# Kernel tuning notes

Measured on AMD Instinct MI355X. Metric: run time of the kernel, lower is better.

The kernel has to match this reference:

```python
import jax, jax.numpy as jnp
import numpy as np

B, L = 4096, 2048
TIMESTEPS = 1000
BETA_START, BETA_END = 1e-4, 0.02


def setup_inputs() -> dict:
    key = jax.random.key(0)
    k0, k1, k2 = jax.random.split(key, 3)
    x_0 = jax.random.normal(k0, (B, L, 2), dtype=jnp.float32)
    t = jax.random.randint(k1, (B,), 0, TIMESTEPS)
    noise = jax.random.normal(k2, (B, L, 2), dtype=jnp.float32)
    return {"x_0": x_0, "t": t, "noise": noise}


def reference(x_0, t, noise):
    # Schedules exactly as in PathDDPM.__init__
    betas = jnp.linspace(BETA_START, BETA_END, TIMESTEPS, dtype=x_0.dtype)
    alphas_cumprod = jnp.cumprod(1.0 - betas)
    sqrt_alphas_cumprod = jnp.sqrt(alphas_cumprod)
    sqrt_one_minus_alphas_cumprod = jnp.sqrt(1.0 - alphas_cumprod)
    # q(x_t | x_0): gather per-sample scalars, broadcast over [L, 2]
    a = sqrt_alphas_cumprod[t][:, None, None]       # [B,1,1]
    s = sqrt_one_minus_alphas_cumprod[t][:, None, None]  # [B,1,1]
    x_t = a * x_0 + s * noise
    return (x_t, noise)
```

## Files before the change

### kernel.cpp

```cpp
#include <hip/hip_runtime.h>
#include <math.h>


#define TSTEPS 1000
#define BSTART 1e-4
#define BEND   0.02

__global__ void ddpm_schedule_kernel(float* __restrict__ ws) {
    const int lane = threadIdx.x;
    const int CHUNK = 16;
    const double step = (BEND - BSTART) / (double)(TSTEPS - 1);
    const int i0 = lane * CHUNK;

    double p = 1.0;
    for (int k = 0; k < CHUNK; ++k) {
        int i = i0 + k;
        if (i < TSTEPS) {
            double beta = BSTART + step * (double)i;
            p *= (1.0 - beta);
        }
    }
    double scan = p;
    #pragma unroll
    for (int off = 1; off < 64; off <<= 1) {
        double o = __shfl_up(scan, off);
        if (lane >= off) scan *= o;
    }
    double excl = __shfl_up(scan, 1);
    if (lane == 0) excl = 1.0;

    double run = excl;
    for (int k = 0; k < CHUNK; ++k) {
        int i = i0 + k;
        if (i < TSTEPS) {
            double beta = BSTART + step * (double)i;
            run *= (1.0 - beta);
            ws[i]          = (float)sqrt(run);
            ws[TSTEPS + i] = (float)sqrt(1.0 - run);
        }
    }
}

__global__ void __launch_bounds__(256)
ddpm_qsample_kernel(const float4* __restrict__ x0,
                    const int*    __restrict__ t,
                    const float4* __restrict__ nz,
                    float4*       __restrict__ out_xt,
                    float4*       __restrict__ out_nz,
                    const float*  __restrict__ ws,
                    int n4) {
    const float* __restrict__ sa = ws;
    const float* __restrict__ ss = ws + TSTEPS;
    const int stride = gridDim.x * blockDim.x;
    for (int i = blockIdx.x * blockDim.x + threadIdx.x; i < n4; i += stride) {
        const int b  = i >> 10;
        const int tb = t[b];
        const float a = sa[tb];
        const float s = ss[tb];
        const float4 x = x0[i];
        const float4 n = nz[i];
        float4 o;
        o.x = fmaf(a, x.x, s * n.x);
        o.y = fmaf(a, x.y, s * n.y);
        o.z = fmaf(a, x.z, s * n.z);
        o.w = fmaf(a, x.w, s * n.w);
        out_xt[i] = o;
        out_nz[i] = n;
    }
}

extern "C" void kernel_launch(void* const* d_in, const int* in_sizes, int n_in,
                              void* d_out, int out_size, void* d_ws, size_t ws_size,
                              hipStream_t stream) {
    const float* x0 = (const float*)d_in[0];
    const int*   t  = (const int*)  d_in[1];
    const float* nz = (const float*)d_in[2];
    float* out = (float*)d_out;
    float* ws  = (float*)d_ws;

    const int n  = 4096 * 2048 * 2;
    const int n4 = n / 4;

    ddpm_schedule_kernel<<<1, 64, 0, stream>>>(ws);
    ddpm_qsample_kernel<<<2048, 256, 0, stream>>>(
        (const float4*)x0, t, (const float4*)nz,
        (float4*)out, (float4*)(out + n), ws, n4);
}
```

Before: 51.16 us.

## Fuse schedule computation into qsample kernel with shared-memory tables and nontemporal stores

Removes the separate single-block schedule kernel: every block now recomputes the cumulative-product tables into shared memory with one wavefront, then runs a fixed 8-iteration unrolled loop. The per-sample index is made wave-uniform with readfirstlane, and outputs are written with nontemporal stores. The aim is to drop one kernel launch and the serialization between the two kernels, and to cut cache pollution on the streaming writes. In exchange each block redundantly runs a double-precision scan before any loads, and the loop bounds are hardcoded to the problem size.

```diff
diff --git a/kernel.cpp b/kernel.cpp
--- a/kernel.cpp
+++ b/kernel.cpp
@@ -6,66 +6,69 @@
 #define BSTART 1e-4
 #define BEND   0.02
 
-__global__ void ddpm_schedule_kernel(float* __restrict__ ws) {
-    const int lane = threadIdx.x;
-    const int CHUNK = 16;
-    const double step = (BEND - BSTART) / (double)(TSTEPS - 1);
-    const int i0 = lane * CHUNK;
+typedef float f4 __attribute__((ext_vector_type(4)));
 
-    double p = 1.0;
-    for (int k = 0; k < CHUNK; ++k) {
-        int i = i0 + k;
-        if (i < TSTEPS) {
-            double beta = BSTART + step * (double)i;
-            p *= (1.0 - beta);
+__global__ void __launch_bounds__(256) ddpm_fused_kernel(
+    const f4*  __restrict__ x0,
+    const int* __restrict__ t,
+    const f4*  __restrict__ nz,
+    f4*        __restrict__ out_xt,
+    f4*        __restrict__ out_nz)
+{
+    __shared__ float s_a[TSTEPS];
+    __shared__ float s_s[TSTEPS];
+
+    if (threadIdx.x < 64) {
+        const int lane = threadIdx.x;
+        const double step = (BEND - BSTART) / (double)(TSTEPS - 1);
+        const int i0 = lane * 16;
+
+        double p = 1.0;
+        #pragma unroll
+        for (int k = 0; k < 16; ++k) {
+            int i = i0 + k;
+            if (i < TSTEPS) p *= (1.0 - (BSTART + step * (double)i));
+        }
+        double scan = p;
+        #pragma unroll
+        for (int off = 1; off < 64; off <<= 1) {
+            double o = __shfl_up(scan, off);
+            if (lane >= off) scan *= o;
+        }
+        double excl = __shfl_up(scan, 1);
+        if (lane == 0) excl = 1.0;
+
+        double run = excl;
+        #pragma unroll
+        for (int k = 0; k < 16; ++k) {
+            int i = i0 + k;
+            if (i < TSTEPS) {
+                run *= (1.0 - (BSTART + step * (double)i));
+                s_a[i] = (float)sqrt(run);
+                s_s[i] = (float)sqrt(1.0 - run);
+            }
         }
     }
-    double scan = p;
+    __syncthreads();
+
+    const int base = blockIdx.x * 256 + threadIdx.x;
     #pragma unroll
-    for (int off = 1; off < 64; off <<= 1) {
-        double o = __shfl_up(scan, off);
-        if (lane >= off) scan *= o;
-    }
-    double excl = __shfl_up(scan, 1);
-    if (lane == 0) excl = 1.0;
+    for (int k = 0; k < 8; ++k) {
+        const int i = base + k * 524288;
+        const int b  = __builtin_amdgcn_readfirstlane(i >> 10);
+        const int tb = t[b];
+        const float a = s_a[tb];
+        const float s = s_s[tb];
 
-    double run = excl;
-    for (int k = 0; k < CHUNK; ++k) {
-        int i = i0 + k;
-        if (i < TSTEPS) {
-            double beta = BSTART + step * (double)i;
-            run *= (1.0 - beta);
-            ws[i]          = (float)sqrt(run);
-            ws[TSTEPS + i] = (float)sqrt(1.0 - run);
-        }
-    }
-}
-
-__global__ void __launch_bounds__(256)
-ddpm_qsample_kernel(const float4* __restrict__ x0,
-                    const int*    __restrict__ t,
-                    const float4* __restrict__ nz,
-                    float4*       __restrict__ out_xt,
-                    float4*       __restrict__ out_nz,
-                    const float*  __restrict__ ws,
-                    int n4) {
-    const float* __restrict__ sa = ws;
-    const float* __restrict__ ss = ws + TSTEPS;
-    const int stride = gridDim.x * blockDim.x;
-    for (int i = blockIdx.x * blockDim.x + threadIdx.x; i < n4; i += stride) {
-        const int b  = i >> 10;
-        const int tb = t[b];
-        const float a = sa[tb];
-        const float s = ss[tb];
-        const float4 x = x0[i];
-        const float4 n = nz[i];
-        float4 o;
+        const f4 x = x0[i];
+        const f4 n = nz[i];
+        f4 o;
         o.x = fmaf(a, x.x, s * n.x);
         o.y = fmaf(a, x.y, s * n.y);
         o.z = fmaf(a, x.z, s * n.z);
         o.w = fmaf(a, x.w, s * n.w);
-        out_xt[i] = o;
-        out_nz[i] = n;
+        __builtin_nontemporal_store(o, &out_xt[i]);
+        __builtin_nontemporal_store(n, &out_nz[i]);
     }
 }
 
@@ -76,13 +79,9 @@
     const int*   t  = (const int*)  d_in[1];
     const float* nz = (const float*)d_in[2];
     float* out = (float*)d_out;
-    float* ws  = (float*)d_ws;
+    const int n = 4096 * 2048 * 2;
 
-    const int n  = 4096 * 2048 * 2;
-    const int n4 = n / 4;
-
-    ddpm_schedule_kernel<<<1, 64, 0, stream>>>(ws);
-    ddpm_qsample_kernel<<<2048, 256, 0, stream>>>(
-        (const float4*)x0, t, (const float4*)nz,
-        (float4*)out, (float4*)(out + n), ws, n4);
+    ddpm_fused_kernel<<<2048, 256, 0, stream>>>(
+        (const f4*)x0, t, (const f4*)nz,
+        (f4*)out, (f4*)(out + n));
 }
```

New measurement: 52.16 us. No clear change (+1.9%).
